# Performance work log

Measured on AMD Instinct MI355X. Metric: run time of the kernel, lower is better.

Reference implementation:

```python
import jax, jax.numpy as jnp
import numpy as np

B, NUNIT_ALL, NCOL = 128, 1024, 8


def setup_inputs() -> dict:
    key = jax.random.key(0)
    k1, k2, k3 = jax.random.split(key, 3)
    x = jax.random.normal(k1, (B, NUNIT_ALL * NUNIT_ALL), dtype=jnp.float32)
    u = jax.random.normal(k2, (NUNIT_ALL // 2, NCOL), dtype=jnp.float32)
    v = jax.random.normal(k3, (NUNIT_ALL // 2, NCOL), dtype=jnp.float32)
    return {"x": x, "u": u, "v": v}


def reference(x, u, v):
    # u, v: (nUnit, ncol); nUnit_all = 2*nUnit
    nunit, ncol = u.shape
    n_all = 2 * nunit
    # normalize u, v jointly by the column norms of concat([u, v], axis=0)
    uv_norm = jnp.linalg.norm(jnp.concatenate([u, v], axis=0), axis=0, keepdims=True)
    un = u / uv_norm
    vn = v / uv_norm
    z = jnp.zeros_like(un)
    uo = jnp.concatenate([un, z], axis=0)   # (n_all, ncol)
    ov = jnp.concatenate([z, vn], axis=0)   # (n_all, ncol)
    b = x.shape[0]
    x3 = x.reshape(b, n_all, n_all)         # per-sample Jacobian J
    # projections J @ uo, J @ ov : (b, n_all, ncol)
    uo_f = jnp.einsum('bij,jc->bic', x3, uo)
    ov_f = jnp.einsum('bij,jc->bic', x3, ov)
    # quadratic forms per column c: (b, ncol)
    uJu = jnp.einsum('ic,bic->bc', uo, uo_f)
    vJu = jnp.einsum('ic,bic->bc', ov, uo_f)
    uJv = jnp.einsum('ic,bic->bc', uo, ov_f)
    vJv = jnp.einsum('ic,bic->bc', ov, ov_f)
    return jnp.concatenate([uJu, vJu, uJv, vJv], axis=-1)  # (b, 4*ncol)
```

## Files before the change

kernel.cpp:

```cpp
#include <hip/hip_runtime.h>

#define NALL 1024
#define NH   512
#define NCOL 8
#define ROWS_PER_BLOCK 64
#define THREADS 256
#define CHUNKS (NALL / ROWS_PER_BLOCK)

typedef float f32x4 __attribute__((ext_vector_type(4)));

__global__ __launch_bounds__(THREADS) void jxy_kernel(
    const float* __restrict__ x, const float* __restrict__ u,
    const float* __restrict__ v, float* __restrict__ out) {
    const int bid   = blockIdx.x;
    const int b     = bid >> 4;
    const int chunk = bid & (CHUNKS - 1);
    const int r0    = chunk * ROWS_PER_BLOCK;
    const int ih    = (r0 >= NH) ? 1 : 0;
    const int rloc  = r0 - ih * NH;

    const int tid  = threadIdx.x;
    const int wave = tid >> 6;
    const int lane = tid & 63;
    const int jbase = wave * 256 + lane * 4;
    const int jh    = (jbase >= NH) ? 1 : 0;
    const int jloc  = jbase - jh * NH;

    __shared__ float red[THREADS];
    __shared__ float inv_norm[NCOL];
    {
        const int c   = tid & 7;
        const int seg = tid >> 3;
        float s = 0.f;
        for (int r = seg; r < NH; r += 32) {
            float a = u[r * NCOL + c];
            float bb = v[r * NCOL + c];
            s = fmaf(a, a, fmaf(bb, bb, s));
        }
        red[tid] = s;
        __syncthreads();
        for (int off = THREADS / 2; off >= NCOL; off >>= 1) {
            if (tid < off) red[tid] += red[tid + off];
            __syncthreads();
        }
        if (tid < NCOL) inv_norm[tid] = 1.0f / sqrtf(red[tid]);
        __syncthreads();
    }

    __shared__ __align__(16) float wl[ROWS_PER_BLOCK * NCOL];
    const float* rawl = ih ? v : u;
    for (int idx = tid; idx < ROWS_PER_BLOCK * NCOL; idx += THREADS)
        wl[idx] = rawl[rloc * NCOL + idx] * inv_norm[idx & 7];

    const float* rawr = jh ? v : u;
    float wr[4][NCOL];
#pragma unroll
    for (int k = 0; k < 4; ++k) {
        const float4* p = reinterpret_cast<const float4*>(rawr + (size_t)(jloc + k) * NCOL);
        float4 a = p[0];
        float4 bq = p[1];
        wr[k][0] = a.x * inv_norm[0];  wr[k][1] = a.y * inv_norm[1];
        wr[k][2] = a.z * inv_norm[2];  wr[k][3] = a.w * inv_norm[3];
        wr[k][4] = bq.x * inv_norm[4]; wr[k][5] = bq.y * inv_norm[5];
        wr[k][6] = bq.z * inv_norm[6]; wr[k][7] = bq.w * inv_norm[7];
    }
    __syncthreads();

    float acc[NCOL];
#pragma unroll
    for (int c = 0; c < NCOL; ++c) acc[c] = 0.f;

    const float* xrow = x + ((size_t)b * NALL + r0) * NALL + jbase;

#pragma unroll 8
    for (int r = 0; r < ROWS_PER_BLOCK; ++r) {
        f32x4 xv = __builtin_nontemporal_load(
            reinterpret_cast<const f32x4*>(xrow + (size_t)r * NALL));

        float t[NCOL];
#pragma unroll
        for (int c = 0; c < NCOL; ++c)
            t[c] = fmaf(xv.x, wr[0][c],
                   fmaf(xv.y, wr[1][c],
                   fmaf(xv.z, wr[2][c],
                        xv.w * wr[3][c])));

        float4 wa = *reinterpret_cast<const float4*>(&wl[r * NCOL]);
        float4 wb = *reinterpret_cast<const float4*>(&wl[r * NCOL + 4]);
        acc[0] = fmaf(wa.x, t[0], acc[0]);
        acc[1] = fmaf(wa.y, t[1], acc[1]);
        acc[2] = fmaf(wa.z, t[2], acc[2]);
        acc[3] = fmaf(wa.w, t[3], acc[3]);
        acc[4] = fmaf(wb.x, t[4], acc[4]);
        acc[5] = fmaf(wb.y, t[5], acc[5]);
        acc[6] = fmaf(wb.z, t[6], acc[6]);
        acc[7] = fmaf(wb.w, t[7], acc[7]);
    }

#pragma unroll
    for (int c = 0; c < NCOL; ++c) {
#pragma unroll
        for (int off = 32; off >= 1; off >>= 1)
            acc[c] += __shfl_xor(acc[c], off, 64);
    }

    if (lane == 0) {
        const int q = ih + 2 * jh;
        float* o = out + (size_t)b * (4 * NCOL) + q * NCOL;
#pragma unroll
        for (int c = 0; c < NCOL; ++c)
            atomicAdd(o + c, acc[c]);
    }
}

extern "C" void kernel_launch(void* const* d_in, const int* in_sizes, int n_in,
                              void* d_out, int out_size, void* d_ws, size_t ws_size,
                              hipStream_t stream) {
    const float* x = (const float*)d_in[0];
    const float* u = (const float*)d_in[1];
    const float* v = (const float*)d_in[2];
    float* out = (float*)d_out;

    const int b_count = in_sizes[0] / (NALL * NALL);

    (void)hipMemsetAsync(d_out, 0, (size_t)out_size * sizeof(float), stream);

    dim3 grid(b_count * CHUNKS);
    jxy_kernel<<<grid, THREADS, 0, stream>>>(x, u, v, out);
}
```

Before: 100.9 us.

## Stream x rows through per-wave LDS ring via async global_load_lds

Replaces direct nontemporal global loads of x with a per-wave 8-deep LDS ring buffer filled by global_load_lds (16-byte direct-to-LDS loads), using explicit vmcnt waits to keep several rows in flight while computing. The aim is deeper memory-level parallelism for this bandwidth-bound streaming kernel. It adds 32KB of LDS per block, which can reduce occupancy, and adds LDS reads. The ring slot is overwritten right after it is read without a wave barrier, which relies on in-order LDS semantics within a wave.

```diff
diff --git a/kernel.cpp b/kernel.cpp
--- a/kernel.cpp
+++ b/kernel.cpp
@@ -1,4 +1,5 @@
 #include <hip/hip_runtime.h>
+#include <stdint.h>
 
 #define NALL 1024
 #define NH   512
@@ -6,8 +7,16 @@
 #define ROWS_PER_BLOCK 64
 #define THREADS 256
 #define CHUNKS (NALL / ROWS_PER_BLOCK)
+#define DEPTH 8
 
 typedef float f32x4 __attribute__((ext_vector_type(4)));
+
+__device__ __forceinline__ void load_to_lds16(const float* gp, float* lds_base) {
+    __builtin_amdgcn_global_load_lds(
+        (const __attribute__((address_space(1))) uint32_t*)gp,
+        (__attribute__((address_space(3))) uint32_t*)lds_base,
+        16, 0, 0);
+}
 
 __global__ __launch_bounds__(THREADS) void jxy_kernel(
     const float* __restrict__ x, const float* __restrict__ u,
@@ -66,36 +75,52 @@
     }
     __syncthreads();
 
+    __shared__ __align__(16) float ring[4][DEPTH][256];
+
     float acc[NCOL];
 #pragma unroll
     for (int c = 0; c < NCOL; ++c) acc[c] = 0.f;
 
     const float* xrow = x + ((size_t)b * NALL + r0) * NALL + jbase;
+    float* ring_base = &ring[wave][0][0];
 
-#pragma unroll 8
-    for (int r = 0; r < ROWS_PER_BLOCK; ++r) {
-        f32x4 xv = __builtin_nontemporal_load(
-            reinterpret_cast<const f32x4*>(xrow + (size_t)r * NALL));
+#pragma unroll
+    for (int s = 0; s < DEPTH; ++s)
+        load_to_lds16(xrow + (size_t)s * NALL, ring_base + s * 256);
 
-        float t[NCOL];
+#define COMPUTE_ROW(r)                                                        \
+    {                                                                         \
+        f32x4 xv = *reinterpret_cast<const f32x4*>(                           \
+            &ring[wave][(r) & (DEPTH - 1)][lane * 4]);                        \
+        float t[NCOL];                                                        \
+        _Pragma("unroll")                                                     \
+        for (int c = 0; c < NCOL; ++c)                                        \
+            t[c] = fmaf(xv.x, wr[0][c],                                       \
+                   fmaf(xv.y, wr[1][c],                                       \
+                   fmaf(xv.z, wr[2][c],                                       \
+                        xv.w * wr[3][c])));                                   \
+        float4 wa = *reinterpret_cast<const float4*>(&wl[(r) * NCOL]);        \
+        float4 wb = *reinterpret_cast<const float4*>(&wl[(r) * NCOL + 4]);    \
+        acc[0] = fmaf(wa.x, t[0], acc[0]);                                    \
+        acc[1] = fmaf(wa.y, t[1], acc[1]);                                    \
+        acc[2] = fmaf(wa.z, t[2], acc[2]);                                    \
+        acc[3] = fmaf(wa.w, t[3], acc[3]);                                    \
+        acc[4] = fmaf(wb.x, t[4], acc[4]);                                    \
+        acc[5] = fmaf(wb.y, t[5], acc[5]);                                    \
+        acc[6] = fmaf(wb.z, t[6], acc[6]);                                    \
+        acc[7] = fmaf(wb.w, t[7], acc[7]);                                    \
+    }
+
+    for (int r = 0; r < ROWS_PER_BLOCK - DEPTH; ++r) {
+        asm volatile("s_waitcnt vmcnt(%0)" :: "i"(DEPTH - 1) : "memory");
+        COMPUTE_ROW(r);
+        load_to_lds16(xrow + (size_t)(r + DEPTH) * NALL,
+                      ring_base + (r & (DEPTH - 1)) * 256);
+    }
+    asm volatile("s_waitcnt vmcnt(0)" ::: "memory");
 #pragma unroll
-        for (int c = 0; c < NCOL; ++c)
-            t[c] = fmaf(xv.x, wr[0][c],
-                   fmaf(xv.y, wr[1][c],
-                   fmaf(xv.z, wr[2][c],
-                        xv.w * wr[3][c])));
-
-        float4 wa = *reinterpret_cast<const float4*>(&wl[r * NCOL]);
-        float4 wb = *reinterpret_cast<const float4*>(&wl[r * NCOL + 4]);
-        acc[0] = fmaf(wa.x, t[0], acc[0]);
-        acc[1] = fmaf(wa.y, t[1], acc[1]);
-        acc[2] = fmaf(wa.z, t[2], acc[2]);
-        acc[3] = fmaf(wa.w, t[3], acc[3]);
-        acc[4] = fmaf(wb.x, t[4], acc[4]);
-        acc[5] = fmaf(wb.y, t[5], acc[5]);
-        acc[6] = fmaf(wb.z, t[6], acc[6]);
-        acc[7] = fmaf(wb.w, t[7], acc[7]);
-    }
+    for (int r = ROWS_PER_BLOCK - DEPTH; r < ROWS_PER_BLOCK; ++r)
+        COMPUTE_ROW(r);
 
 #pragma unroll
     for (int c = 0; c < NCOL; ++c) {
```

Result: slower. 126.7 us (+25.6%).

## Use one 1024-thread block per batch half and drop atomics and memset

Applied to the files above, without the earlier changes.

Restructures the grid so each 1024-thread block covers a full half of a batch sample's rows, with 16 waves splitting rows and column quarters. Partial sums are reduced in shared memory and written directly, which removes the output memset launch and the global atomics. The cost is far fewer blocks (one per CU), so latency hiding rests on 16 waves per block, and the per-block norm reduction and weight staging now run over a larger shared buffer.

```diff
diff --git a/kernel.cpp b/kernel.cpp
--- a/kernel.cpp
+++ b/kernel.cpp
@@ -3,28 +3,27 @@
 #define NALL 1024
 #define NH   512
 #define NCOL 8
-#define ROWS_PER_BLOCK 64
-#define THREADS 256
-#define CHUNKS (NALL / ROWS_PER_BLOCK)
+#define THREADS 1024
+#define ROWS_PER_WAVE 128
 
 typedef float f32x4 __attribute__((ext_vector_type(4)));
 
 __global__ __launch_bounds__(THREADS) void jxy_kernel(
     const float* __restrict__ x, const float* __restrict__ u,
     const float* __restrict__ v, float* __restrict__ out) {
-    const int bid   = blockIdx.x;
-    const int b     = bid >> 4;
-    const int chunk = bid & (CHUNKS - 1);
-    const int r0    = chunk * ROWS_PER_BLOCK;
-    const int ih    = (r0 >= NH) ? 1 : 0;
-    const int rloc  = r0 - ih * NH;
+    const int bid = blockIdx.x;
+    const int b   = bid >> 1;
+    const int ih  = bid & 1;
+    const int r0  = ih * NH;
 
     const int tid  = threadIdx.x;
     const int wave = tid >> 6;
     const int lane = tid & 63;
-    const int jbase = wave * 256 + lane * 4;
-    const int jh    = (jbase >= NH) ? 1 : 0;
-    const int jloc  = jbase - jh * NH;
+    const int wg   = wave >> 2;
+    const int jq   = wave & 3;
+    const int jh   = jq >> 1;
+    const int jbase = jq * 256 + lane * 4;
+    const int jloc  = (jq & 1) * 256 + lane * 4;
 
     __shared__ float red[THREADS];
     __shared__ float inv_norm[NCOL];
@@ -32,7 +31,7 @@
         const int c   = tid & 7;
         const int seg = tid >> 3;
         float s = 0.f;
-        for (int r = seg; r < NH; r += 32) {
+        for (int r = seg; r < NH; r += 128) {
             float a = u[r * NCOL + c];
             float bb = v[r * NCOL + c];
             s = fmaf(a, a, fmaf(bb, bb, s));
@@ -47,10 +46,10 @@
         __syncthreads();
     }
 
-    __shared__ __align__(16) float wl[ROWS_PER_BLOCK * NCOL];
+    __shared__ __align__(16) float wl[NH * NCOL];
     const float* rawl = ih ? v : u;
-    for (int idx = tid; idx < ROWS_PER_BLOCK * NCOL; idx += THREADS)
-        wl[idx] = rawl[rloc * NCOL + idx] * inv_norm[idx & 7];
+    for (int idx = tid; idx < NH * NCOL; idx += THREADS)
+        wl[idx] = rawl[idx] * inv_norm[idx & 7];
 
     const float* rawr = jh ? v : u;
     float wr[4][NCOL];
@@ -70,10 +69,12 @@
 #pragma unroll
     for (int c = 0; c < NCOL; ++c) acc[c] = 0.f;
 
-    const float* xrow = x + ((size_t)b * NALL + r0) * NALL + jbase;
+    const int rw = wg * ROWS_PER_WAVE;
+    const float* xrow = x + ((size_t)b * NALL + r0 + rw) * NALL + jbase;
+    const float* wlw  = &wl[rw * NCOL];
 
 #pragma unroll 8
-    for (int r = 0; r < ROWS_PER_BLOCK; ++r) {
+    for (int r = 0; r < ROWS_PER_WAVE; ++r) {
         f32x4 xv = __builtin_nontemporal_load(
             reinterpret_cast<const f32x4*>(xrow + (size_t)r * NALL));
 
@@ -85,8 +86,8 @@
                    fmaf(xv.z, wr[2][c],
                         xv.w * wr[3][c])));
 
-        float4 wa = *reinterpret_cast<const float4*>(&wl[r * NCOL]);
-        float4 wb = *reinterpret_cast<const float4*>(&wl[r * NCOL + 4]);
+        float4 wa = *reinterpret_cast<const float4*>(&wlw[r * NCOL]);
+        float4 wb = *reinterpret_cast<const float4*>(&wlw[r * NCOL + 4]);
         acc[0] = fmaf(wa.x, t[0], acc[0]);
         acc[1] = fmaf(wa.y, t[1], acc[1]);
         acc[2] = fmaf(wa.z, t[2], acc[2]);
@@ -104,12 +105,25 @@
             acc[c] += __shfl_xor(acc[c], off, 64);
     }
 
+    __shared__ float part[16][NCOL];
     if (lane == 0) {
-        const int q = ih + 2 * jh;
-        float* o = out + (size_t)b * (4 * NCOL) + q * NCOL;
 #pragma unroll
-        for (int c = 0; c < NCOL; ++c)
-            atomicAdd(o + c, acc[c]);
+        for (int c = 0; c < NCOL; ++c) part[wave][c] = acc[c];
+    }
+    __syncthreads();
+
+    if (tid < 16) {
+        const int jh_sel = tid >> 3;
+        const int c      = tid & 7;
+        float s = 0.f;
+#pragma unroll
+        for (int wgi = 0; wgi < 4; ++wgi) {
+#pragma unroll
+            for (int jqi = 0; jqi < 2; ++jqi)
+                s += part[wgi * 4 + jh_sel * 2 + jqi][c];
+        }
+        const int q = ih + 2 * jh_sel;
+        out[(size_t)b * (4 * NCOL) + q * NCOL + c] = s;
     }
 }
 
@@ -123,8 +137,6 @@
 
     const int b_count = in_sizes[0] / (NALL * NALL);
 
-    (void)hipMemsetAsync(d_out, 0, (size_t)out_size * sizeof(float), stream);
-
-    dim3 grid(b_count * CHUNKS);
+    dim3 grid(b_count * 2);
     jxy_kernel<<<grid, THREADS, 0, stream>>>(x, u, v, out);
 }
```

After: 87.62 us. 13.1% less time.
